# Kernel tuning notes

Hardware: AMD Instinct MI355X
Metric: run time of the kernel (lower is better)

Reference implementation:

```python
import jax, jax.numpy as jnp
import numpy as np

H = 8        # num_heads
LN_EPS = 1e-5
NEG = -1000000.0


def setup_inputs() -> dict:
    key = jax.random.key(0)
    ks = jax.random.split(key, 8)
    B, T, D = 4, 4096, 1024
    s = 1.0 / np.sqrt(D)
    x = jax.random.normal(ks[0], (B, T, D), dtype=jnp.float32)
    tmask = (jnp.arange(T) < (3 * T) // 4).astype(jnp.float32)
    src_mask = jnp.broadcast_to(tmask[None, :, None], (B, T, 1)).astype(jnp.float32)
    Wq = jax.random.normal(ks[1], (D, D), dtype=jnp.float32) * s
    Wk = jax.random.normal(ks[2], (D, D), dtype=jnp.float32) * s
    Wv = jax.random.normal(ks[3], (D, D), dtype=jnp.float32) * s
    bq = jnp.zeros((D,), jnp.float32)
    bk = jnp.zeros((D,), jnp.float32)
    bv = jnp.zeros((D,), jnp.float32)
    gamma = jnp.ones((D,), jnp.float32)
    beta = jnp.zeros((D,), jnp.float32)
    return {"x": x, "src_mask": src_mask, "Wq": Wq, "bq": bq, "Wk": Wk,
            "bk": bk, "Wv": Wv, "bv": bv, "gamma": gamma, "beta": beta}


def reference(x, src_mask, Wq, bq, Wk, bk, Wv, bv, gamma, beta):
    B, T, D = x.shape
    Dh = D // H
    # LayerNorm (same normed input feeds q, k, v)
    mu = jnp.mean(x, axis=-1, keepdims=True)
    var = jnp.mean(jnp.square(x - mu), axis=-1, keepdims=True)
    xn = (x - mu) * jax.lax.rsqrt(var + LN_EPS) * gamma + beta
    q = xn @ Wq + bq                               # [B,T,D]
    k = xn @ Wk + bk + (1.0 - src_mask) * NEG      # mask padded timesteps
    v = (xn @ Wv + bv) * src_mask                  # zero padded values
    q = jax.nn.softmax(q.reshape(B, T, H, Dh), axis=-1)   # over feature dim
    k = jax.nn.softmax(k.reshape(B, T, H, Dh), axis=1)    # over time dim
    v = v.reshape(B, T, H, Dh)
    # efficient/linear attention: O(T * Dh^2) per head
    att = jnp.einsum('bnhd,bnhl->bhdl', k, v)      # [B,H,Dh,Dh]
    y = jnp.einsum('bnhd,bhdl->bnhl', q, att).reshape(B, T, D)
    return x + y
```

## Files before the change

kernel.cpp:

```cpp
#include <hip/hip_runtime.h>
#include <stdint.h>


typedef unsigned short u16;
typedef __attribute__((ext_vector_type(8))) short bf16x8;
typedef __attribute__((ext_vector_type(4))) float f32x4;

__device__ u16 g_WT[3][1024 * 1024];
__device__ u16 g_xn[16777216];
__device__ float g_attp[8388608];
__device__ u16 g_attT[524288];
__device__ float g_Z[4096];
__device__ int g_mflag[64];

__device__ __forceinline__ float b2f(u16 u) {
  union { unsigned int i; float f; } c;
  c.i = ((unsigned int)u) << 16;
  return c.f;
}
__device__ __forceinline__ u16 f2b(float f) {
  union { float f; unsigned int i; } c;
  c.f = f;
  unsigned int r = c.i + 0x7fffu + ((c.i >> 16) & 1u);
  return (u16)(r >> 16);
}

__device__ __forceinline__ void gload16(const void* g, void* l) {
  __builtin_amdgcn_global_load_lds(
      reinterpret_cast<const __attribute__((address_space(1))) uint32_t*>(
          reinterpret_cast<uintptr_t>(g)),
      reinterpret_cast<__attribute__((address_space(3))) uint32_t*>(
          reinterpret_cast<uintptr_t>(l)),
      16, 0, 0);
}

__device__ __forceinline__ void stageA256(char* buf, const u16* gsrc, int h,
                                          int wave, int lane) {
#pragma unroll
  for (int i = 0; i < 2; i++) {
    const int ib = i * 64 + wave * 8;
    const int rowb = (ib & 63) | ((ib & 64) << 1) | (h << 6);
    const int row = rowb + (lane >> 3);
    const int cc = (lane & 7) ^ (row & 7);
    gload16((const char*)gsrc + ((size_t)row * 1024 + cc * 8) * 2,
            buf + rowb * 128);
  }
}
__device__ __forceinline__ void stageB256(char* buf, const u16* gsrc, int h,
                                          int wave, int lane) {
#pragma unroll
  for (int i = 0; i < 2; i++) {
    const int ib = i * 64 + wave * 8;
    const int rowb = (ib & 31) | ((ib & 96) << 1) | (h << 5);
    const int row = rowb + (lane >> 3);
    const int cc = (lane & 7) ^ (row & 7);
    gload16((const char*)gsrc + ((size_t)row * 1024 + cc * 8) * 2,
            buf + rowb * 128);
  }
}
__device__ __forceinline__ void stageC128(char* buf, const u16* gsrc,
                                          int wave, int lane) {
#pragma unroll
  for (int i = 0; i < 2; i++) {
    const int rowb = i * 64 + wave * 8;
    const int row = rowb + (lane >> 3);
    const int cc = (lane & 7) ^ (row & 7);
    gload16((const char*)gsrc + ((size_t)row * 1024 + cc * 8) * 2,
            buf + rowb * 128);
  }
}
__device__ __forceinline__ bf16x8 fragS(const char* buf, int R, int ks, int lane) {
  const int q = lane >> 4;
  return *(const bf16x8*)(buf + R * 128 + ((((ks << 2) + q) ^ (R & 7)) << 4));
}

template <bool ST>
__device__ __forceinline__ void tile_1ph(char* Ab, char* Bb, char* An, char* Bn,
                                         const u16* Agn, const u16* Bgn,
                                         f32x4 (&acc)[8][4], int wave, int lane,
                                         int wm, int wn) {
  if constexpr (ST) {
    stageA256(An, Agn, 0, wave, lane);
    stageA256(An, Agn, 1, wave, lane);
    stageB256(Bn, Bgn, 0, wave, lane);
    stageB256(Bn, Bgn, 1, wave, lane);
  }
  bf16x8 a[4][2], b[4][2];
#pragma unroll
  for (int cf = 0; cf < 4; cf++) {
    const int R = wn * 64 + cf * 16 + (lane & 15);
#pragma unroll
    for (int ks = 0; ks < 2; ks++) b[cf][ks] = fragS(Bb, R, ks, lane);
  }
#pragma unroll
  for (int rf = 0; rf < 4; rf++) {
    const int R = wm * 128 + rf * 16 + (lane & 15);
#pragma unroll
    for (int ks = 0; ks < 2; ks++) a[rf][ks] = fragS(Ab, R, ks, lane);
  }
  __builtin_amdgcn_s_setprio(1);
#pragma unroll
  for (int rf = 0; rf < 4; rf++)
#pragma unroll
    for (int cf = 0; cf < 4; cf++)
#pragma unroll
      for (int ks = 0; ks < 2; ks++)
        acc[rf][cf] = __builtin_amdgcn_mfma_f32_16x16x32_bf16(
            a[rf][ks], b[cf][ks], acc[rf][cf], 0, 0, 0);
  bf16x8 a2[4][2];
#pragma unroll
  for (int rf = 0; rf < 4; rf++) {
    const int R = wm * 128 + 64 + rf * 16 + (lane & 15);
#pragma unroll
    for (int ks = 0; ks < 2; ks++) a2[rf][ks] = fragS(Ab, R, ks, lane);
  }
#pragma unroll
  for (int rf = 0; rf < 4; rf++)
#pragma unroll
    for (int cf = 0; cf < 4; cf++)
#pragma unroll
      for (int ks = 0; ks < 2; ks++)
        acc[4 + rf][cf] = __builtin_amdgcn_mfma_f32_16x16x32_bf16(
            a2[rf][ks], b[cf][ks], acc[4 + rf][cf], 0, 0, 0);
  __builtin_amdgcn_s_setprio(0);
  if constexpr (ST) asm volatile("s_waitcnt vmcnt(0)" ::: "memory");
  __builtin_amdgcn_s_barrier();
  __builtin_amdgcn_sched_barrier(0);
}

template <bool ST>
__device__ __forceinline__ void tile_kv(char* Ab, char* Bkb, char* Bvb,
                                        char* An, char* Bkn, char* Bvn,
                                        const u16* Agn, const u16* Bkgn,
                                        const u16* Bvgn, f32x4 (&ae)[8][2],
                                        f32x4 (&av)[8][2], int wave, int lane,
                                        int wm, int wn) {
  if constexpr (ST) {
    stageA256(An, Agn, 0, wave, lane);
    stageA256(An, Agn, 1, wave, lane);
    stageC128(Bkn, Bkgn, wave, lane);
    stageC128(Bvn, Bvgn, wave, lane);
  }
  bf16x8 bk[2][2], bv[2][2];
#pragma unroll
  for (int cf = 0; cf < 2; cf++) {
    const int R = wn * 32 + cf * 16 + (lane & 15);
#pragma unroll
    for (int ks = 0; ks < 2; ks++) {
      bk[cf][ks] = fragS(Bkb, R, ks, lane);
      bv[cf][ks] = fragS(Bvb, R, ks, lane);
    }
  }
  bf16x8 a[4][2];
#pragma unroll
  for (int rf = 0; rf < 4; rf++) {
    const int R = wm * 128 + rf * 16 + (lane & 15);
#pragma unroll
    for (int ks = 0; ks < 2; ks++) a[rf][ks] = fragS(Ab, R, ks, lane);
  }
  __builtin_amdgcn_s_setprio(1);
#pragma unroll
  for (int rf = 0; rf < 4; rf++)
#pragma unroll
    for (int cf = 0; cf < 2; cf++)
#pragma unroll
      for (int ks = 0; ks < 2; ks++) {
        ae[rf][cf] = __builtin_amdgcn_mfma_f32_16x16x32_bf16(
            a[rf][ks], bk[cf][ks], ae[rf][cf], 0, 0, 0);
        av[rf][cf] = __builtin_amdgcn_mfma_f32_16x16x32_bf16(
            a[rf][ks], bv[cf][ks], av[rf][cf], 0, 0, 0);
      }
  bf16x8 a2[4][2];
#pragma unroll
  for (int rf = 0; rf < 4; rf++) {
    const int R = wm * 128 + 64 + rf * 16 + (lane & 15);
#pragma unroll
    for (int ks = 0; ks < 2; ks++) a2[rf][ks] = fragS(Ab, R, ks, lane);
  }
#pragma unroll
  for (int rf = 0; rf < 4; rf++)
#pragma unroll
    for (int cf = 0; cf < 2; cf++)
#pragma unroll
      for (int ks = 0; ks < 2; ks++) {
        ae[4 + rf][cf] = __builtin_amdgcn_mfma_f32_16x16x32_bf16(
            a2[rf][ks], bk[cf][ks], ae[4 + rf][cf], 0, 0, 0);
        av[4 + rf][cf] = __builtin_amdgcn_mfma_f32_16x16x32_bf16(
            a2[rf][ks], bv[cf][ks], av[4 + rf][cf], 0, 0, 0);
      }
  __builtin_amdgcn_s_setprio(0);
  if constexpr (ST) asm volatile("s_waitcnt vmcnt(0)" ::: "memory");
  __builtin_amdgcn_s_barrier();
  __builtin_amdgcn_sched_barrier(0);
}

__global__ __launch_bounds__(256) void prep_kernel(const float* __restrict__ x,
                                                   const float* __restrict__ gamma,
                                                   const float* __restrict__ beta,
                                                   const float* __restrict__ wq,
                                                   const float* __restrict__ wk,
                                                   const float* __restrict__ wv,
                                                   const float* __restrict__ mask) {
  __shared__ float ls[4], ls2[4];
  __shared__ u16 tile[32][33];
  __shared__ int sflag;
  const int bid = blockIdx.x;
  const int tid = threadIdx.x;
  if (bid < 16384) {
    if (bid < 16) g_Z[bid * 256 + tid] = 0.0f;
    if (bid < 64) {
      if (tid == 0) sflag = 0;
      __syncthreads();
      if (mask[bid * 256 + tid] > 0.5f) atomicOr(&sflag, 1);
      __syncthreads();
      if (tid == 0) g_mflag[bid] = sflag;
    }
    const int wave = tid >> 6, lane = tid & 63;
    const float* xr = x + (size_t)bid * 1024;
    float4 u = ((const float4*)xr)[tid];
    float v0 = u.x, v1 = u.y, v2 = u.z, v3 = u.w;
    float s = v0 + v1 + v2 + v3;
    float s2 = v0 * v0 + v1 * v1 + v2 * v2 + v3 * v3;
#pragma unroll
    for (int off = 32; off > 0; off >>= 1) {
      s += __shfl_down(s, off);
      s2 += __shfl_down(s2, off);
    }
    if (lane == 0) { ls[wave] = s; ls2[wave] = s2; }
    __syncthreads();
    s = ls[0] + ls[1] + ls[2] + ls[3];
    s2 = ls2[0] + ls2[1] + ls2[2] + ls2[3];
    const float mu = s * (1.0f / 1024.0f);
    const float var = fmaxf(s2 * (1.0f / 1024.0f) - mu * mu, 0.0f);
    const float rstd = rsqrtf(var + 1e-5f);
    float4 g4 = ((const float4*)gamma)[tid];
    float4 be = ((const float4*)beta)[tid];
    ushort4 o;
    o.x = f2b((v0 - mu) * rstd * g4.x + be.x);
    o.y = f2b((v1 - mu) * rstd * g4.y + be.y);
    o.z = f2b((v2 - mu) * rstd * g4.z + be.z);
    o.w = f2b((v3 - mu) * rstd * g4.w + be.w);
    *(ushort4*)(g_xn + (size_t)bid * 1024 + tid * 4) = o;
  } else {
    const int id = bid - 16384;
    const int which = id >> 10;
    const int rem = id & 1023;
    const float* src = (which == 0) ? wq : (which == 1) ? wk : wv;
    u16* dst = g_WT[which];
    const int tx = tid & 31;
    const int ty = tid >> 5;
    const int c0 = (rem & 31) * 32, r0 = (rem >> 5) * 32;
#pragma unroll
    for (int i = 0; i < 4; i++)
      tile[ty + i * 8][tx] = f2b(src[(size_t)(r0 + ty + i * 8) * 1024 + c0 + tx]);
    __syncthreads();
#pragma unroll
    for (int i = 0; i < 4; i++)
      dst[(size_t)(c0 + ty + i * 8) * 1024 + r0 + tx] = tile[tx][ty + i * 8];
  }
}

__global__ __launch_bounds__(512, 2) void gemm_kva(const float* __restrict__ bk,
                                                   const float* __restrict__ bv,
                                                   const float* __restrict__ mask) {
  __shared__ __align__(16) char smem[131072];
  const int tid = threadIdx.x, wave = tid >> 6, lane = tid & 63;
  const int L = blockIdx.x;
  const int bt = L & 63;
  const int h = L >> 6;
  const int m0 = bt * 256;
  const int b = m0 >> 12;
  const int tt = bt & 15;
  if (!g_mflag[bt]) return;

  const int wm = wave >> 2, wn = wave & 3;
  const u16* Ag = g_xn + (size_t)m0 * 1024;
  const u16* Bkg = g_WT[1] + (size_t)(h * 128) * 1024;
  const u16* Bvg = g_WT[2] + (size_t)(h * 128) * 1024;

  char* A0 = smem;
  char* Bk0 = smem + 32768;
  char* Bv0 = smem + 49152;
  char* A1 = smem + 65536;
  char* Bk1 = smem + 98304;
  char* Bv1 = smem + 114688;

  f32x4 zero = {0.f, 0.f, 0.f, 0.f};
  f32x4 ae[8][2], av[8][2];
#pragma unroll
  for (int i = 0; i < 8; i++)
#pragma unroll
    for (int j = 0; j < 2; j++) { ae[i][j] = zero; av[i][j] = zero; }

  stageA256(A0, Ag, 0, wave, lane);
  stageA256(A0, Ag, 1, wave, lane);
  stageC128(Bk0, Bkg, wave, lane);
  stageC128(Bv0, Bvg, wave, lane);
  asm volatile("s_waitcnt vmcnt(0)" ::: "memory");
  __builtin_amdgcn_s_barrier();

#pragma unroll 1
  for (int t = 0; t < 15; ++t) {
    const int p = t & 1;
    tile_kv<true>(p ? A1 : A0, p ? Bk1 : Bk0, p ? Bv1 : Bv0,
                  p ? A0 : A1, p ? Bk0 : Bk1, p ? Bv0 : Bv1,
                  Ag + (t + 1) * 64, Bkg + (t + 1) * 64, Bvg + (t + 1) * 64,
                  ae, av, wave, lane, wm, wn);
  }
  tile_kv<false>(A1, Bk1, Bv1, A0, Bk0, Bv0, Ag, Bkg, Bvg, ae, av, wave, lane,
                 wm, wn);

  u16* ekT = (u16*)smem;
  u16* vvT = (u16*)(smem + 65536);
  float fsum[2] = {0.f, 0.f};
#pragma unroll
  for (int rf = 0; rf < 8; rf++)
#pragma unroll
    for (int r = 0; r < 4; r++) {
      const int tok = wm * 128 + rf * 16 + (lane >> 4) * 4 + r;
      const float mv = mask[m0 + tok];
#pragma unroll
      for (int cf = 0; cf < 2; cf++) {
        const int feat = wn * 32 + cf * 16 + (lane & 15);
        const int slot = (((tok >> 3) ^ (feat & 31)) << 3) | (tok & 7);
        const float ve = ae[rf][cf][r] + bk[h * 128 + feat];
        const float oe = (mv > 0.5f) ? __expf(fminf(ve, 30.0f)) : 0.0f;
        const u16 eb = f2b(oe);
        ekT[feat * 256 + slot] = eb;
        fsum[cf] += b2f(eb);
        const float vv = (av[rf][cf][r] + bv[h * 128 + feat]) * mv;
        vvT[feat * 256 + slot] = f2b(vv);
      }
    }
#pragma unroll
  for (int cf = 0; cf < 2; cf++) {
    float s = fsum[cf];
    s += __shfl_xor(s, 16);
    s += __shfl_xor(s, 32);
    if (lane < 16)
      atomicAdd(&g_Z[b * 1024 + h * 128 + wn * 32 + cf * 16 + lane], s);
  }
  __syncthreads();

  f32x4 acc2[4][2];
#pragma unroll
  for (int i = 0; i < 4; i++)
#pragma unroll
    for (int j = 0; j < 2; j++) acc2[i][j] = zero;
#pragma unroll
  for (int ks = 0; ks < 8; ks++) {
    bf16x8 aF[4], bF[2];
#pragma unroll
    for (int rf = 0; rf < 4; rf++) {
      const int d = wm * 64 + rf * 16 + (lane & 15);
      aF[rf] = *(const bf16x8*)&ekT[d * 256 +
          ((((ks << 2) + (lane >> 4)) ^ (d & 31)) << 3)];
    }
#pragma unroll
    for (int cf = 0; cf < 2; cf++) {
      const int l = wn * 32 + cf * 16 + (lane & 15);
      bF[cf] = *(const bf16x8*)&vvT[l * 256 +
          ((((ks << 2) + (lane >> 4)) ^ (l & 31)) << 3)];
    }
#pragma unroll
    for (int rf = 0; rf < 4; rf++)
#pragma unroll
      for (int cf = 0; cf < 2; cf++)
        acc2[rf][cf] = __builtin_amdgcn_mfma_f32_16x16x32_bf16(
            aF[rf], bF[cf], acc2[rf][cf], 0, 0, 0);
  }

  float* op = g_attp + (size_t)(tt * 32 + b * 8 + h) * 16384;
#pragma unroll
  for (int rf = 0; rf < 4; rf++)
#pragma unroll
    for (int r = 0; r < 4; r++) {
      const int d = wm * 64 + rf * 16 + (lane >> 4) * 4 + r;
#pragma unroll
      for (int cf = 0; cf < 2; cf++) {
        const int l = wn * 32 + cf * 16 + (lane & 15);
        op[d * 128 + l] = acc2[rf][cf][r];
      }
    }
}

__global__ __launch_bounds__(256) void attnorm_kernel() {
  const int bh = blockIdx.x;
  const int b = bh >> 3, h = bh & 7;
  const int tid = threadIdx.x;
  __shared__ float Zl[128];
  __shared__ int vfl[16];
  if (tid < 128) Zl[tid] = fmaxf(g_Z[b * 1024 + h * 128 + tid], 1e-30f);
  if (tid < 16) vfl[tid] = g_mflag[b * 16 + tid];
  __syncthreads();
  const int i0 = blockIdx.y * 2048;
  for (int i = i0 + tid; i < i0 + 2048; i += 256) {
    const int d = i >> 7, l = i & 127;
    float s = 0.f;
#pragma unroll
    for (int c = 0; c < 16; c++)
      if (vfl[c]) s += g_attp[((size_t)(c * 32 + bh)) * 16384 + i];
    g_attT[(size_t)bh * 16384 + l * 128 + d] = f2b(s / Zl[d]);
  }
}

__global__ __launch_bounds__(512, 2) void gemm_qy(const float* __restrict__ bq,
                                                  const float* __restrict__ x,
                                                  float* __restrict__ out) {
  __shared__ __align__(16) char smem[131072];
  __shared__ float zq4[4][256];
  const int tid = threadIdx.x, wave = tid >> 6, lane = tid & 63;
  const int L = blockIdx.x;
  const int g = L >> 3;
  const int mt = (L & 7) + 8 * (g >> 2);
  const int n0 = (g & 3) * 256;
  const int m0 = mt * 256;
  const int b = m0 >> 12;
  const int wm = wave >> 2, wn = wave & 3;
  const u16* Ag = g_xn + (size_t)m0 * 1024;
  const u16* Bg = g_WT[0] + (size_t)n0 * 1024;

  f32x4 zero = {0.f, 0.f, 0.f, 0.f};
  f32x4 acc[8][4];
#pragma unroll
  for (int i = 0; i < 8; i++)
#pragma unroll
    for (int j = 0; j < 4; j++) acc[i][j] = zero;

  stageA256(smem, Ag, 0, wave, lane);
  stageA256(smem, Ag, 1, wave, lane);
  stageB256(smem + 65536, Bg, 0, wave, lane);
  stageB256(smem + 65536, Bg, 1, wave, lane);
  asm volatile("s_waitcnt vmcnt(0)" ::: "memory");
  __builtin_amdgcn_s_barrier();

#pragma unroll 1
  for (int t = 0; t < 15; ++t) {
    const int p = t & 1;
    tile_1ph<true>(smem + p * 32768, smem + 65536 + p * 32768,
                   smem + (p ^ 1) * 32768, smem + 65536 + (p ^ 1) * 32768,
                   Ag + (t + 1) * 64, Bg + (t + 1) * 64, acc, wave, lane, wm, wn);
  }
  tile_1ph<false>(smem + 32768, smem + 65536 + 32768, smem, smem + 65536, Ag,
                  Bg, acc, wave, lane, wm, wn);

  const int hl = wn >> 1;
  const int bhh = b * 8 + (n0 >> 7) + hl;
  const u16* attb = g_attT + ((size_t)bhh << 14);
  bf16x8 bpre[4][4];
#pragma unroll
  for (int ks = 0; ks < 4; ks++)
#pragma unroll
    for (int cf = 0; cf < 4; cf++) {
      const int l = (wn & 1) * 64 + cf * 16 + (lane & 15);
      bpre[ks][cf] = *(const bf16x8*)(attb + l * 128 + ks * 32 + (lane >> 4) * 8);
    }

  u16* qs = (u16*)smem;
#pragma unroll
  for (int rf = 0; rf < 8; rf++)
#pragma unroll
    for (int r = 0; r < 4; r++) {
      const int tok = wm * 128 + rf * 16 + (lane >> 4) * 4 + r;
      float rs = 0.f;
#pragma unroll
      for (int cf = 0; cf < 4; cf++) {
        const int f = wn * 64 + cf * 16 + (lane & 15);
        const float e = __expf(fminf(acc[rf][cf][r] + bq[n0 + f], 30.0f));
        qs[tok * 256 + ((((f >> 3) ^ (tok & 31)) << 3) | (f & 7))] = f2b(e);
        rs += e;
      }
      rs += __shfl_xor(rs, 1);
      rs += __shfl_xor(rs, 2);
      rs += __shfl_xor(rs, 4);
      rs += __shfl_xor(rs, 8);
      if ((lane & 15) == 0) zq4[wn][tok] = rs;
    }
  __syncthreads();

  f32x4 acc2[8][4];
#pragma unroll
  for (int i = 0; i < 8; i++)
#pragma unroll
    for (int j = 0; j < 4; j++) acc2[i][j] = zero;

#pragma unroll
  for (int ks = 0; ks < 4; ks++) {
    bf16x8 af[8];
#pragma unroll
    for (int rf = 0; rf < 8; rf++) {
      const int tok = wm * 128 + rf * 16 + (lane & 15);
      af[rf] = *(const bf16x8*)&qs[tok * 256 +
          ((((hl << 4) + (ks << 2) + (lane >> 4)) ^ (tok & 31)) << 3)];
    }
#pragma unroll
    for (int rf = 0; rf < 8; rf++)
#pragma unroll
      for (int cf = 0; cf < 4; cf++)
        acc2[rf][cf] = __builtin_amdgcn_mfma_f32_16x16x32_bf16(
            af[rf], bpre[ks][cf], acc2[rf][cf], 0, 0, 0);
  }

#pragma unroll
  for (int rf = 0; rf < 8; rf++)
#pragma unroll
    for (int r = 0; r < 4; r++) {
      const int tok = wm * 128 + rf * 16 + (lane >> 4) * 4 + r;
      const float zq =
          fmaxf(zq4[hl * 2][tok] + zq4[hl * 2 + 1][tok], 1e-30f);
      const size_t n = (size_t)(m0 + tok);
#pragma unroll
      for (int cf = 0; cf < 4; cf++) {
        const int f = wn * 64 + cf * 16 + (lane & 15);
        const size_t idx = n * 1024 + n0 + f;
        out[idx] = x[idx] + acc2[rf][cf][r] / zq;
      }
    }
}

extern "C" void kernel_launch(void* const* d_in, const int* in_sizes, int n_in,
                              void* d_out, int out_size, void* d_ws, size_t ws_size,
                              hipStream_t stream) {
  const float* x = (const float*)d_in[0];
  const float* mask = (const float*)d_in[1];
  const float* Wq = (const float*)d_in[2];
  const float* bq = (const float*)d_in[3];
  const float* Wk = (const float*)d_in[4];
  const float* bk = (const float*)d_in[5];
  const float* Wv = (const float*)d_in[6];
  const float* bv = (const float*)d_in[7];
  const float* gamma = (const float*)d_in[8];
  const float* beta = (const float*)d_in[9];
  float* out = (float*)d_out;
  (void)d_ws; (void)ws_size;

  prep_kernel<<<dim3(16384 + 3072), 256, 0, stream>>>(x, gamma, beta, Wq, Wk, Wv, mask);
  gemm_kva<<<dim3(512), 512, 0, stream>>>(bk, bv, mask);
  attnorm_kernel<<<dim3(32, 8), 256, 0, stream>>>();
  gemm_qy<<<dim3(256), 512, 0, stream>>>(bq, x, out);
}
```

Before: 320.1 us.

## Pre-swizzle weights into MFMA fragment layout and load B directly from global

The weight-transpose prep kernel now writes Wq/Wk/Wv in a per-head, per-k-tile MFMA fragment order. The GEMM kernels read B fragments straight from global/L2 with 16-byte vector loads instead of staging them through LDS. This drops B staging traffic and LDS use in the main loops. B loads now sit on the critical path with no double buffering, so global/L2 latency may stall the MFMAs.

```diff
diff --git a/kernel.cpp b/kernel.cpp
--- a/kernel.cpp
+++ b/kernel.cpp
@@ -6,7 +6,7 @@
 typedef __attribute__((ext_vector_type(8))) short bf16x8;
 typedef __attribute__((ext_vector_type(4))) float f32x4;
 
-__device__ u16 g_WT[3][1024 * 1024];
+__device__ u16 g_WF[3][1024 * 1024];
 __device__ u16 g_xn[16777216];
 __device__ float g_attp[8388608];
 __device__ u16 g_attT[524288];
@@ -46,51 +46,32 @@
             buf + rowb * 128);
   }
 }
-__device__ __forceinline__ void stageB256(char* buf, const u16* gsrc, int h,
-                                          int wave, int lane) {
-#pragma unroll
-  for (int i = 0; i < 2; i++) {
-    const int ib = i * 64 + wave * 8;
-    const int rowb = (ib & 31) | ((ib & 96) << 1) | (h << 5);
-    const int row = rowb + (lane >> 3);
-    const int cc = (lane & 7) ^ (row & 7);
-    gload16((const char*)gsrc + ((size_t)row * 1024 + cc * 8) * 2,
-            buf + rowb * 128);
-  }
-}
-__device__ __forceinline__ void stageC128(char* buf, const u16* gsrc,
-                                          int wave, int lane) {
-#pragma unroll
-  for (int i = 0; i < 2; i++) {
-    const int rowb = i * 64 + wave * 8;
-    const int row = rowb + (lane >> 3);
-    const int cc = (lane & 7) ^ (row & 7);
-    gload16((const char*)gsrc + ((size_t)row * 1024 + cc * 8) * 2,
-            buf + rowb * 128);
-  }
-}
 __device__ __forceinline__ bf16x8 fragS(const char* buf, int R, int ks, int lane) {
   const int q = lane >> 4;
   return *(const bf16x8*)(buf + R * 128 + ((((ks << 2) + q) ^ (R & 7)) << 4));
 }
+__device__ __forceinline__ bf16x8 fragW(const u16* wf, int t, int ks, int fb,
+                                        int lane) {
+  return *(const bf16x8*)(wf + (size_t)(((t * 2 + ks) * 8) + fb) * 512 +
+                          lane * 8);
+}
 
 template <bool ST>
-__device__ __forceinline__ void tile_1ph(char* Ab, char* Bb, char* An, char* Bn,
-                                         const u16* Agn, const u16* Bgn,
+__device__ __forceinline__ void tile_1ph(char* Ab, char* An, const u16* Agn,
+                                         const u16* wfQ, int hbase, int t,
                                          f32x4 (&acc)[8][4], int wave, int lane,
                                          int wm, int wn) {
   if constexpr (ST) {
     stageA256(An, Agn, 0, wave, lane);
     stageA256(An, Agn, 1, wave, lane);
-    stageB256(Bn, Bgn, 0, wave, lane);
-    stageB256(Bn, Bgn, 1, wave, lane);
   }
   bf16x8 a[4][2], b[4][2];
 #pragma unroll
   for (int cf = 0; cf < 4; cf++) {
-    const int R = wn * 64 + cf * 16 + (lane & 15);
-#pragma unroll
-    for (int ks = 0; ks < 2; ks++) b[cf][ks] = fragS(Bb, R, ks, lane);
+    const int fc = wn * 4 + cf;
+    const u16* wf = wfQ + (size_t)(hbase + (fc >> 3)) * 131072;
+#pragma unroll
+    for (int ks = 0; ks < 2; ks++) b[cf][ks] = fragW(wf, t, ks, fc & 7, lane);
   }
 #pragma unroll
   for (int rf = 0; rf < 4; rf++) {
@@ -129,26 +110,22 @@
 }
 
 template <bool ST>
-__device__ __forceinline__ void tile_kv(char* Ab, char* Bkb, char* Bvb,
-                                        char* An, char* Bkn, char* Bvn,
-                                        const u16* Agn, const u16* Bkgn,
-                                        const u16* Bvgn, f32x4 (&ae)[8][2],
-                                        f32x4 (&av)[8][2], int wave, int lane,
-                                        int wm, int wn) {
+__device__ __forceinline__ void tile_kv(char* Ab, char* An, const u16* Agn,
+                                        const u16* wfK, const u16* wfV, int t,
+                                        f32x4 (&ae)[8][2], f32x4 (&av)[8][2],
+                                        int wave, int lane, int wm, int wn) {
   if constexpr (ST) {
     stageA256(An, Agn, 0, wave, lane);
     stageA256(An, Agn, 1, wave, lane);
-    stageC128(Bkn, Bkgn, wave, lane);
-    stageC128(Bvn, Bvgn, wave, lane);
   }
   bf16x8 bk[2][2], bv[2][2];
 #pragma unroll
   for (int cf = 0; cf < 2; cf++) {
-    const int R = wn * 32 + cf * 16 + (lane & 15);
+    const int fb = wn * 2 + cf;
 #pragma unroll
     for (int ks = 0; ks < 2; ks++) {
-      bk[cf][ks] = fragS(Bkb, R, ks, lane);
-      bv[cf][ks] = fragS(Bvb, R, ks, lane);
+      bk[cf][ks] = fragW(wfK, t, ks, fb, lane);
+      bv[cf][ks] = fragW(wfV, t, ks, fb, lane);
     }
   }
   bf16x8 a[4][2];
@@ -246,7 +223,6 @@
     const int which = id >> 10;
     const int rem = id & 1023;
     const float* src = (which == 0) ? wq : (which == 1) ? wk : wv;
-    u16* dst = g_WT[which];
     const int tx = tid & 31;
     const int ty = tid >> 5;
     const int c0 = (rem & 31) * 32, r0 = (rem >> 5) * 32;
@@ -254,9 +230,18 @@
     for (int i = 0; i < 4; i++)
       tile[ty + i * 8][tx] = f2b(src[(size_t)(r0 + ty + i * 8) * 1024 + c0 + tx]);
     __syncthreads();
-#pragma unroll
-    for (int i = 0; i < 4; i++)
-      dst[(size_t)(c0 + ty + i * 8) * 1024 + r0 + tx] = tile[tx][ty + i * 8];
+    if (tid < 128) {
+      const int f_loc = tid & 31, jg = tid >> 5;
+      const int f = c0 + f_loc, kd0 = r0 + jg * 8;
+      const int h = f >> 7, fb = (f >> 4) & 7, r = f & 15;
+      const int t = kd0 >> 6, ks = (kd0 >> 5) & 1, q = (kd0 >> 3) & 3;
+      union { u16 u[8]; uint4 v; } pk;
+#pragma unroll
+      for (int j = 0; j < 8; j++) pk.u[j] = tile[jg * 8 + j][f_loc];
+      const size_t off =
+          ((size_t)((((h * 16 + t) * 2 + ks) * 8 + fb)) * 64 + q * 16 + r) * 8;
+      *(uint4*)&g_WF[which][off] = pk.v;
+    }
   }
 }
 
@@ -275,15 +260,11 @@
 
   const int wm = wave >> 2, wn = wave & 3;
   const u16* Ag = g_xn + (size_t)m0 * 1024;
-  const u16* Bkg = g_WT[1] + (size_t)(h * 128) * 1024;
-  const u16* Bvg = g_WT[2] + (size_t)(h * 128) * 1024;
+  const u16* wfK = g_WF[1] + (size_t)h * 131072;
+  const u16* wfV = g_WF[2] + (size_t)h * 131072;
 
   char* A0 = smem;
-  char* Bk0 = smem + 32768;
-  char* Bv0 = smem + 49152;
-  char* A1 = smem + 65536;
-  char* Bk1 = smem + 98304;
-  char* Bv1 = smem + 114688;
+  char* A1 = smem + 32768;
 
   f32x4 zero = {0.f, 0.f, 0.f, 0.f};
   f32x4 ae[8][2], av[8][2];
@@ -294,21 +275,16 @@
 
   stageA256(A0, Ag, 0, wave, lane);
   stageA256(A0, Ag, 1, wave, lane);
-  stageC128(Bk0, Bkg, wave, lane);
-  stageC128(Bv0, Bvg, wave, lane);
   asm volatile("s_waitcnt vmcnt(0)" ::: "memory");
   __builtin_amdgcn_s_barrier();
 
 #pragma unroll 1
   for (int t = 0; t < 15; ++t) {
     const int p = t & 1;
-    tile_kv<true>(p ? A1 : A0, p ? Bk1 : Bk0, p ? Bv1 : Bv0,
-                  p ? A0 : A1, p ? Bk0 : Bk1, p ? Bv0 : Bv1,
-                  Ag + (t + 1) * 64, Bkg + (t + 1) * 64, Bvg + (t + 1) * 64,
-                  ae, av, wave, lane, wm, wn);
-  }
-  tile_kv<false>(A1, Bk1, Bv1, A0, Bk0, Bv0, Ag, Bkg, Bvg, ae, av, wave, lane,
-                 wm, wn);
+    tile_kv<true>(p ? A1 : A0, p ? A0 : A1, Ag + (t + 1) * 64, wfK, wfV, t, ae,
+                  av, wave, lane, wm, wn);
+  }
+  tile_kv<false>(A1, A0, Ag, wfK, wfV, 15, ae, av, wave, lane, wm, wn);
 
   u16* ekT = (u16*)smem;
   u16* vvT = (u16*)(smem + 65536);
@@ -416,9 +392,13 @@
   const int n0 = (g & 3) * 256;
   const int m0 = mt * 256;
   const int b = m0 >> 12;
+  const int hbase = n0 >> 7;
   const int wm = wave >> 2, wn = wave & 3;
   const u16* Ag = g_xn + (size_t)m0 * 1024;
-  const u16* Bg = g_WT[0] + (size_t)n0 * 1024;
+  const u16* wfQ = g_WF[0];
+
+  char* A0 = smem;
+  char* A1 = smem + 32768;
 
   f32x4 zero = {0.f, 0.f, 0.f, 0.f};
   f32x4 acc[8][4];
@@ -427,22 +407,18 @@
 #pragma unroll
     for (int j = 0; j < 4; j++) acc[i][j] = zero;
 
-  stageA256(smem, Ag, 0, wave, lane);
-  stageA256(smem, Ag, 1, wave, lane);
-  stageB256(smem + 65536, Bg, 0, wave, lane);
-  stageB256(smem + 65536, Bg, 1, wave, lane);
+  stageA256(A0, Ag, 0, wave, lane);
+  stageA256(A0, Ag, 1, wave, lane);
   asm volatile("s_waitcnt vmcnt(0)" ::: "memory");
   __builtin_amdgcn_s_barrier();
 
 #pragma unroll 1
   for (int t = 0; t < 15; ++t) {
     const int p = t & 1;
-    tile_1ph<true>(smem + p * 32768, smem + 65536 + p * 32768,
-                   smem + (p ^ 1) * 32768, smem + 65536 + (p ^ 1) * 32768,
-                   Ag + (t + 1) * 64, Bg + (t + 1) * 64, acc, wave, lane, wm, wn);
-  }
-  tile_1ph<false>(smem + 32768, smem + 65536 + 32768, smem, smem + 65536, Ag,
-                  Bg, acc, wave, lane, wm, wn);
+    tile_1ph<true>(p ? A1 : A0, p ? A0 : A1, Ag + (t + 1) * 64, wfQ, hbase, t,
+                   acc, wave, lane, wm, wn);
+  }
+  tile_1ph<false>(A1, A0, Ag, wfQ, hbase, 15, acc, wave, lane, wm, wn);
 
   const int hl = wn >> 1;
   const int bhh = b * 8 + (n0 >> 7) + hl;
```

New measurement: 332.4 us. 1.04x slower.
